# Kernel tuning notes

Measured on AMD Instinct MI355X. Metric: run time of the kernel, lower is better.

## Reference

```python
import jax, jax.numpy as jnp
import numpy as np

MAX_PER_CLASS = 100   # max_num_boxes_per_class
MAX_TOTAL = 300       # max_num_boxes (pad_per_class=False -> output size is MAX_TOTAL)
IOU_THR = 0.5
SCORE_THR = 0.001
NEG = jnp.float32(-1e30)
EPS = 1e-12


def _canon(b):
    # boxes given as any diagonal pair (y1,x1,y2,x2); canonicalize like TF NMS
    ymin = jnp.minimum(b[..., 0], b[..., 2])
    ymax = jnp.maximum(b[..., 0], b[..., 2])
    xmin = jnp.minimum(b[..., 1], b[..., 3])
    xmax = jnp.maximum(b[..., 1], b[..., 3])
    return ymin, xmin, ymax, xmax


def _iou_one_vs_all(box, boxes):
    # box [4], boxes [N,4] -> iou [N]
    y1a, x1a, y2a, x2a = _canon(box)
    y1b, x1b, y2b, x2b = _canon(boxes)
    ih = jnp.maximum(jnp.minimum(y2a, y2b) - jnp.maximum(y1a, y1b), 0.0)
    iw = jnp.maximum(jnp.minimum(x2a, x2b) - jnp.maximum(x1a, x1b), 0.0)
    inter = ih * iw
    area_a = (y2a - y1a) * (x2a - x1a)
    area_b = (y2b - y1b) * (x2b - x1b)
    union = jnp.maximum(area_a + area_b - inter, EPS)
    return inter / union


def _nms_single_class(boxes_c, scores_c):
    # boxes_c [N,4], scores_c [N] -> (scores [K], boxes [K,4], valid [K]) with K=MAX_PER_CLASS
    N = scores_c.shape[0]
    valid = scores_c > SCORE_THR
    s = jnp.where(valid, scores_c, NEG)
    order = jnp.argsort(-s)
    b_sorted = boxes_c[order]          # [N,4]
    s_sorted = s[order]                # [N]
    v_sorted = valid[order]            # [N]

    def step(keep, xs):
        i, box_i, valid_i = xs
        iou_row = _iou_one_vs_all(box_i, b_sorted)          # [N]
        suppressed = jnp.any(keep & (iou_row > IOU_THR))    # vs previously kept only
        keep = keep.at[i].set(valid_i & jnp.logical_not(suppressed))
        return keep, None

    keep0 = jnp.zeros((N,), dtype=bool)
    keep, _ = jax.lax.scan(step, keep0, (jnp.arange(N), b_sorted, v_sorted))

    # cap number of kept boxes at MAX_PER_CLASS (in descending score order)
    rank = jnp.cumsum(keep.astype(jnp.int32)) - 1
    keep = keep & (rank < MAX_PER_CLASS)

    key = jnp.where(keep, s_sorted, NEG)
    top_s, top_i = jax.lax.top_k(key, MAX_PER_CLASS)
    top_boxes = b_sorted[top_i]
    top_valid = top_s > (NEG / 2)
    return top_s, top_boxes, top_valid


def _combined_nms(scores, boxes):
    # scores [B,N,C], boxes [B,N,q,4] with q==1 (boxes shared across classes)
    B, N, C = scores.shape
    q = boxes.shape[2]

    def per_image(scores_i, boxes_i):
        # scores_i [N,C], boxes_i [N,q,4]
        if q == 1:
            cls_boxes = jnp.broadcast_to(boxes_i, (N, C, 4))
        else:
            cls_boxes = boxes_i
        # per-class NMS, vmapped over the class axis
        sc, bx, vd = jax.vmap(_nms_single_class, in_axes=(1, 1))(cls_boxes, scores_i)
        # sc [C,K], bx [C,K,4], vd [C,K]
        cls_ids = jnp.broadcast_to(
            jnp.arange(C, dtype=scores.dtype)[:, None], vd.shape)

        flat_s = jnp.where(vd, sc, NEG).reshape(-1)   # [C*K]
        flat_b = bx.reshape(-1, 4)
        flat_c = cls_ids.reshape(-1)
        flat_v = vd.reshape(-1)

        top_s, idx = jax.lax.top_k(flat_s, MAX_TOTAL)
        out_v = flat_v[idx]
        out_s = jnp.where(out_v, top_s, 0.0)
        out_b = jnp.where(out_v[:, None], flat_b[idx], 0.0)
        out_b = jnp.clip(out_b, 0.0, 1.0)             # clip_boxes=True
        out_c = jnp.where(out_v, flat_c[idx], 0.0)
        count = jnp.sum(out_v.astype(jnp.int32))
        return out_s, out_b, out_c, count

    return jax.vmap(per_image)(scores, boxes)


def setup_inputs() -> dict:
    key = jax.random.key(0)
    k1, k2 = jax.random.split(key)
    B, N, C, Q = 4, 1024, 80, 1
    scores = jax.random.uniform(k1, (B, N, C), dtype=jnp.float32)
    boxes = jax.random.uniform(k2, (B, N, Q, 4), dtype=jnp.float32)
    return {"scores": scores, "boxes": boxes}


def reference(scores, boxes):
    # returns (output_scores, output_boxes, output_classes, valid_counts)
    return _combined_nms(scores, boxes)
```

## Files before the change

### kernel.cpp

```cpp
#include <hip/hip_runtime.h>
#include <stdint.h>

#define N_BOX 1024
#define C_CLS 80
#define B_IMG 4
#define K_PER 100
#define K_TOT 300
#define NEGF  (-1e30f)
#define NWORD 16
#define NCAND (C_CLS * K_PER)
#define M_SEL 8192
#define KPAD  1088

#define OFF_SCOREST 0
#define OFF_MASKS   1310720
#define OFF_WSCORE  1835008
#define OFF_WSIDX   1963008

typedef unsigned long long u64;
typedef unsigned int u32;

__device__ __forceinline__ int swz(int i) { return i + (i >> 4); }

__device__ __forceinline__ u32 ford(float f) {
    u32 u = __float_as_uint(f);
    return (u & 0x80000000u) ? ~u : (u | 0x80000000u);
}
__device__ __forceinline__ float funord(u32 o) {
    u32 u = (o & 0x80000000u) ? (o ^ 0x80000000u) : ~o;
    return __uint_as_float(u);
}

__global__ __launch_bounds__(256) void prep_kernel(
        const float* __restrict__ scores,
        const float* __restrict__ boxes,
        u64*   __restrict__ masks,
        float* __restrict__ scoresT)
{
    __shared__ float4 bx[N_BOX];
    __shared__ float  ar[N_BOX];
    const int tid = threadIdx.x;

    if (blockIdx.x < 256) {
        const int b  = blockIdx.x >> 6;
        const int rg = blockIdx.x & 63;
        for (int n = tid; n < N_BOX; n += 256) {
            float4 v = ((const float4*)boxes)[b * N_BOX + n];
            {
#pragma clang fp contract(off)
                float y1 = fminf(v.x, v.z), y2 = fmaxf(v.x, v.z);
                float x1 = fminf(v.y, v.w), x2 = fmaxf(v.y, v.w);
                bx[n] = make_float4(y1, x1, y2, x2);
                ar[n] = (y2 - y1) * (x2 - x1);
            }
        }
        __syncthreads();

        const int r = tid >> 4;
        const int w = tid & 15;
        const int i = rg * 16 + r;
        const float4 a = bx[i];
        const float area_a = ar[i];
        u64 m = 0;
        const int j0 = w * 64;
        for (int jj = 0; jj < 64; ++jj) {
            int j = j0 + jj;
            float4 q = bx[j];
            {
#pragma clang fp contract(off)
                float ih = fminf(a.z, q.z) - fmaxf(a.x, q.x); ih = fmaxf(ih, 0.0f);
                float iw = fminf(a.w, q.w) - fmaxf(a.y, q.y); iw = fmaxf(iw, 0.0f);
                float inter = ih * iw;
                float uni = fmaxf(area_a + ar[j] - inter, 1e-12f);
                if (j != i && (inter / uni) > 0.5f) m |= (1ull << jj);
            }
        }
        masks[((size_t)(b * N_BOX + i)) * NWORD + w] = m;
    } else {
        float* tile = (float*)bx;
        const int t = blockIdx.x - 256;
        const int b  = t / 320;
        const int rm = t % 320;
        const int n0 = (rm / 5) * 16;
        const int c0 = (rm % 5) * 16;
        const int r = tid >> 4, cc = tid & 15;
        tile[r * 17 + cc] = scores[(size_t)(b * N_BOX + n0 + r) * C_CLS + c0 + cc];
        __syncthreads();
        scoresT[(size_t)(b * C_CLS + c0 + r) * N_BOX + n0 + cc] = tile[cc * 17 + r];
    }
}

__global__ __launch_bounds__(512) void nms_classes(
        const float* __restrict__ scoresT,
        const u64*   __restrict__ masks,
        float* __restrict__ ws_score,
        int*   __restrict__ ws_idx)
{
    __shared__ u64 key[2][KPAD];
    __shared__ u64 rows[2][64][NWORD];
    __shared__ int kept_t[2][K_PER];
    __shared__ int sh_nvalid[2], sh_kept[2];

    const int tid  = threadIdx.x;
    const int half = tid >> 8;
    const int lt   = tid & 255;
    const int lane = tid & 63;
    const int b  = blockIdx.x / (C_CLS / 2);
    const int c  = (blockIdx.x % (C_CLS / 2)) * 2 + half;

    if (lt == 0) { sh_nvalid[half] = 0; sh_kept[half] = 0; }
    __syncthreads();

    u64 r[4];
    {
        const float4 s4 = ((const float4*)(scoresT + ((size_t)(b * C_CLS + c) << 10)))[lt];
        float sv[4] = {s4.x, s4.y, s4.z, s4.w};
        int lv = 0;
        #pragma unroll
        for (int q = 0; q < 4; ++q) {
            bool valid = sv[q] > 0.001f;
            float s = valid ? sv[q] : NEGF;
            int v = lt * 4 + q;
            r[q] = ((u64)ford(s) << 32) | (u32)(N_BOX - 1 - v);
            lv += valid ? 1 : 0;
        }
        if (lv) atomicAdd(&sh_nvalid[half], lv);
    }

    #define CE(a, b, d) { u64 _mx = (a) > (b) ? (a) : (b); \
                          u64 _mn = (a) > (b) ? (b) : (a); \
                          (a) = (d) ? _mx : _mn; (b) = (d) ? _mn : _mx; }
    CE(r[0], r[1], true); CE(r[2], r[3], false);

    for (int k = 4; k <= N_BOX; k <<= 1) {
        const bool d = ((lt & (k >> 2)) == 0);
        for (int j = k >> 1; j > 0; j >>= 1) {
            if (j >= 256) {
                __syncthreads();
                #pragma unroll
                for (int q = 0; q < 4; ++q) key[half][swz(lt * 4 + q)] = r[q];
                __syncthreads();
                const bool upper = ((lt * 4) & j) != 0;
                #pragma unroll
                for (int q = 0; q < 4; ++q) {
                    u64 pv = key[half][swz((lt * 4 + q) ^ j)];
                    u64 mx = r[q] > pv ? r[q] : pv;
                    u64 mn = r[q] > pv ? pv : r[q];
                    r[q] = (d != upper) ? mx : mn;
                }
            } else if (j >= 4) {
                const int dl = j >> 2;
                const bool upper = (lane & dl) != 0;
                #pragma unroll
                for (int q = 0; q < 4; ++q) {
                    u64 pv = __shfl_xor(r[q], dl);
                    u64 mx = r[q] > pv ? r[q] : pv;
                    u64 mn = r[q] > pv ? pv : r[q];
                    r[q] = (d != upper) ? mx : mn;
                }
            } else if (j == 2) {
                CE(r[0], r[2], d); CE(r[1], r[3], d);
            } else {
                CE(r[0], r[1], d); CE(r[2], r[3], d);
            }
        }
    }
    #undef CE

    __syncthreads();
    #pragma unroll
    for (int q = 0; q < 4; ++q) key[half][swz(lt * 4 + q)] = r[q];
    __syncthreads();

    const int wv = tid >> 6;
    if (wv == 0 || wv == 4) {
        const int gh = wv >> 2;
        const int w16 = lane & 15;
        const int sslot = lane >> 4;
        const u64* mrow = masks + (size_t)b * N_BOX * NWORD;
        const int nvalid = sh_nvalid[gh];
        u64 sup = 0;
        int kept = 0;

        for (int bt = 0; bt < nvalid && kept < K_PER; bt += 64) {
            int t = bt + lane;
            bool in = t < nvalid;
            u64 kv = key[gh][swz(t & (N_BOX - 1))];
            int idx = (N_BOX - 1) - (int)(u32)(kv & 0xFFFFFFFFu);
            const int widx = idx >> 6, bidx = idx & 63;

            u64 supw = __shfl(sup, widx);
            bool sbit = (supw >> bidx) & 1ull;
            u64 pending = __ballot(in && !sbit);
            if (!pending) continue;

            #pragma unroll
            for (int p = 0; p < 16; ++p) {
                int rr = p * 4 + sslot;
                int ir = __shfl(idx, rr);
                u64 w = ((bt + rr) < nvalid) ? mrow[(size_t)ir * NWORD + w16] : 0;
                rows[gh][rr][w16] = w;
            }
            __builtin_amdgcn_wave_barrier();

            u64 kill_mask = 0;
            #pragma unroll
            for (int rr = 0; rr < 64; ++rr) {
                u64 w = rows[gh][rr][widx];
                kill_mask |= ((w >> bidx) & 1ull) << rr;
            }

            while (pending && kept < K_PER) {
                int t0 = __ffsll((long long)pending) - 1;
                if (lane == 0) kept_t[gh][kept] = bt + t0;
                kept++;
                if (lane < NWORD) sup |= rows[gh][t0][w16];
                bool kill = (kill_mask >> t0) & 1ull;
                pending &= ~(1ull << t0);
                pending &= ~__ballot(kill);
            }
        }
        if (lane == 0) sh_kept[gh] = kept;
    }
    __syncthreads();

    const int kept = sh_kept[half];
    if (lt < K_PER) {
        int ob = (b * C_CLS + c) * K_PER + lt;
        if (lt < kept) {
            u64 k = key[half][swz(kept_t[half][lt])];
            ws_score[ob] = funord((u32)(k >> 32));
            ws_idx[ob]   = (N_BOX - 1) - (int)(u32)(k & 0xFFFFFFFFu);
        } else {
            ws_score[ob] = NEGF;
            ws_idx[ob]   = 0;
        }
    }
}

__global__ __launch_bounds__(1024) void final_topk(
        const float* __restrict__ ws_score,
        const int*   __restrict__ ws_idx,
        const float* __restrict__ boxes,
        float* __restrict__ out)
{
    __shared__ u32 skey[NCAND];
    __shared__ u32 hist4[256 * 4];
    __shared__ u64 list[512];
    __shared__ int sh_sel;
    __shared__ u32 sh_need;
    __shared__ int sh_cnt, sh_valid;

    const int tid = threadIdx.x;
    const int b = blockIdx.x;
    const int base = b * NCAND;

    if (tid == 0) { sh_cnt = 0; sh_valid = 0; }
    for (int i = tid; i < NCAND; i += 1024)
        skey[i] = ford(ws_score[base + i]);
    if (tid < 512) list[tid] = 0;
    hist4[tid] = 0;
    __syncthreads();

    u64 prefix = 0;
    u32 need = K_TOT;
    const int rounds[6] = {7, 6, 5, 4, 1, 0};
    const int slot = tid & 3;

    for (int rd = 0; rd < 6; ++rd) {
        const int d = rounds[rd];
        for (int i = tid; i < NCAND; i += 1024) {
            u64 k = ((u64)skey[i] << 32) | (u32)(M_SEL - 1 - i);
            bool match = (d == 7) || (((k ^ prefix) >> (8 * (d + 1))) == 0);
            if (match)
                atomicAdd(&hist4[(((u32)(k >> (8 * d)) & 0xFFu) << 2) | slot], 1u);
        }
        __syncthreads();
        if (tid < 64) {
            const int l = tid;
            u32 h[4];
            #pragma unroll
            for (int q = 0; q < 4; ++q) {
                int bin = 4 * l + q;
                h[q] = hist4[bin * 4 + 0] + hist4[bin * 4 + 1]
                     + hist4[bin * 4 + 2] + hist4[bin * 4 + 3];
                hist4[bin * 4 + 0] = 0; hist4[bin * 4 + 1] = 0;
                hist4[bin * 4 + 2] = 0; hist4[bin * 4 + 3] = 0;
            }
            u32 s3 = h[3], s2 = h[2] + s3, s1 = h[1] + s2, s0 = h[0] + s1;
            u32 tot = s0, S = tot;
            #pragma unroll
            for (int off = 1; off < 64; off <<= 1) {
                u32 t = __shfl(S, (l + off) & 63);
                if (l + off < 64) S += t;
            }
            u32 T = S - tot;
            u32 sv0 = s0 + T, sv1 = s1 + T, sv2 = s2 + T, sv3 = s3 + T;
            if (sv0 >= need && sv1 < need) { sh_sel = 4*l;     sh_need = need - sv1; }
            if (sv1 >= need && sv2 < need) { sh_sel = 4*l + 1; sh_need = need - sv2; }
            if (sv2 >= need && sv3 < need) { sh_sel = 4*l + 2; sh_need = need - sv3; }
            if (sv3 >= need && T   < need) { sh_sel = 4*l + 3; sh_need = need - T;   }
        }
        __syncthreads();
        prefix |= ((u64)(u32)sh_sel) << (8 * d);
        need = sh_need;
        __syncthreads();
    }

    for (int i = tid; i < NCAND; i += 1024) {
        u64 k = ((u64)skey[i] << 32) | (u32)(M_SEL - 1 - i);
        if (k >= prefix) {
            int p = atomicAdd(&sh_cnt, 1);
            if (p < 512) list[p] = k;
        }
    }
    __syncthreads();

    if (tid < 64) {
        const int l = tid;
        u64 e[8];
        #pragma unroll
        for (int q = 0; q < 8; ++q) e[q] = list[l * 8 + q];
        #define CE2(a, b, dd) { u64 _mx = (a) > (b) ? (a) : (b); \
                                u64 _mn = (a) > (b) ? (b) : (a); \
                                (a) = (dd) ? _mx : _mn; (b) = (dd) ? _mn : _mx; }
        CE2(e[0], e[1], true);  CE2(e[2], e[3], false);
        CE2(e[4], e[5], true);  CE2(e[6], e[7], false);
        CE2(e[0], e[2], true);  CE2(e[1], e[3], true);
        CE2(e[4], e[6], false); CE2(e[5], e[7], false);
        CE2(e[0], e[1], true);  CE2(e[2], e[3], true);
        CE2(e[4], e[5], false); CE2(e[6], e[7], false);
        for (int k = 8; k <= 512; k <<= 1) {
            const bool d = ((l & (k >> 3)) == 0);
            for (int j = k >> 1; j >= 8; j >>= 1) {
                const int dl = j >> 3;
                const bool upper = (l & dl) != 0;
                #pragma unroll
                for (int q = 0; q < 8; ++q) {
                    u64 pv = __shfl_xor(e[q], dl);
                    u64 mx = e[q] > pv ? e[q] : pv;
                    u64 mn = e[q] > pv ? pv : e[q];
                    e[q] = (d != upper) ? mx : mn;
                }
            }
            CE2(e[0], e[4], d); CE2(e[1], e[5], d);
            CE2(e[2], e[6], d); CE2(e[3], e[7], d);
            CE2(e[0], e[2], d); CE2(e[1], e[3], d);
            CE2(e[4], e[6], d); CE2(e[5], e[7], d);
            CE2(e[0], e[1], d); CE2(e[2], e[3], d);
            CE2(e[4], e[5], d); CE2(e[6], e[7], d);
        }
        #undef CE2
        #pragma unroll
        for (int q = 0; q < 8; ++q) list[l * 8 + q] = e[q];
    }
    __syncthreads();

    float* out_s = out;
    float* out_b = out + B_IMG * K_TOT;
    float* out_c = out + B_IMG * K_TOT * 5;
    float* out_n = out + B_IMG * K_TOT * 6;

    for (int i = tid; i < K_TOT; i += 1024) {
        u64 k = list[i];
        float s = funord((u32)(k >> 32));
        int flat = (M_SEL - 1) - (int)(u32)(k & 0xFFFFFFFFu);
        bool valid = s > (-5e29f);
        float os = 0.0f, oc = 0.0f;
        float4 ob = make_float4(0.0f, 0.0f, 0.0f, 0.0f);
        if (valid && flat < NCAND) {
            int cc = flat / K_PER;
            int n  = ws_idx[base + flat];
            float4 bb = ((const float4*)boxes)[b * N_BOX + n];
            os = s;
            oc = (float)cc;
            ob.x = fminf(fmaxf(bb.x, 0.0f), 1.0f);
            ob.y = fminf(fmaxf(bb.y, 0.0f), 1.0f);
            ob.z = fminf(fmaxf(bb.z, 0.0f), 1.0f);
            ob.w = fminf(fmaxf(bb.w, 0.0f), 1.0f);
            atomicAdd(&sh_valid, 1);
        }
        out_s[b * K_TOT + i] = os;
        ((float4*)out_b)[b * K_TOT + i] = ob;
        out_c[b * K_TOT + i] = oc;
    }
    __syncthreads();
    if (tid == 0) out_n[b] = (float)sh_valid;
}

extern "C" void kernel_launch(void* const* d_in, const int* in_sizes, int n_in,
                              void* d_out, int out_size, void* d_ws, size_t ws_size,
                              hipStream_t stream) {
    const float* scores = (const float*)d_in[0];
    const float* boxes  = (const float*)d_in[1];

    char* ws = (char*)d_ws;
    float* scoresT  = (float*)(ws + OFF_SCOREST);
    u64*   masks    = (u64*)  (ws + OFF_MASKS);
    float* ws_score = (float*)(ws + OFF_WSCORE);
    int*   ws_idx   = (int*)  (ws + OFF_WSIDX);

    prep_kernel<<<dim3(256 + 1280), dim3(256), 0, stream>>>(scores, boxes, masks, scoresT);
    nms_classes<<<dim3(B_IMG * (C_CLS / 2)), dim3(512), 0, stream>>>(
        scoresT, masks, ws_score, ws_idx);
    final_topk<<<dim3(B_IMG), dim3(1024), 0, stream>>>(
        ws_score, ws_idx, boxes, (float*)d_out);
}
```

Before: 131.0 us.

## Precompute per-tile kill masks across all waves before serial NMS scan

Moves the gather of IoU mask rows and the 64x64 in-tile kill-mask construction out of the serial single-wave NMS loop. All four waves per class build these masks for every 64-box tile in parallel and store them in shared memory. The serial wave then only reads the precomputed mask and ORs suppression words for kept boxes, gathering them directly from global memory in batches of eight. This adds work for tiles the serial scan would have skipped and uses more shared memory, which may lower occupancy.

After: 141.0 us. 7.7% more time.

```diff
diff --git a/kernel.cpp b/kernel.cpp
--- a/kernel.cpp
+++ b/kernel.cpp
@@ -97,7 +97,8 @@
         int*   __restrict__ ws_idx)
 {
     __shared__ u64 key[2][KPAD];
-    __shared__ u64 rows[2][64][NWORD];
+    __shared__ u64 killm[2][16][64];
+    __shared__ u64 scratch[2][4][64][NWORD];
     __shared__ int kept_t[2][K_PER];
     __shared__ int sh_nvalid[2], sh_kept[2];
 
@@ -172,52 +173,86 @@
     for (int q = 0; q < 4; ++q) key[half][swz(lt * 4 + q)] = r[q];
     __syncthreads();
 
-    const int wv = tid >> 6;
-    if (wv == 0 || wv == 4) {
-        const int gh = wv >> 2;
-        const int w16 = lane & 15;
-        const int sslot = lane >> 4;
-        const u64* mrow = masks + (size_t)b * N_BOX * NWORD;
-        const int nvalid = sh_nvalid[gh];
-        u64 sup = 0;
-        int kept = 0;
-
-        for (int bt = 0; bt < nvalid && kept < K_PER; bt += 64) {
-            int t = bt + lane;
-            bool in = t < nvalid;
-            u64 kv = key[gh][swz(t & (N_BOX - 1))];
+    const u64* mrow = masks + (size_t)b * N_BOX * NWORD;
+    const int w16 = lane & 15;
+    const int sslot = lane >> 4;
+    const int nvalid = sh_nvalid[half];
+
+    {
+        const int wq = (tid >> 6) & 3;
+        for (int w = wq; w < 16; w += 4) {
+            const int bt = w * 64;
+            if (bt >= nvalid) break;
+            u64 kv = key[half][swz(bt + lane)];
             int idx = (N_BOX - 1) - (int)(u32)(kv & 0xFFFFFFFFu);
             const int widx = idx >> 6, bidx = idx & 63;
-
-            u64 supw = __shfl(sup, widx);
-            bool sbit = (supw >> bidx) & 1ull;
-            u64 pending = __ballot(in && !sbit);
-            if (!pending) continue;
-
             #pragma unroll
             for (int p = 0; p < 16; ++p) {
                 int rr = p * 4 + sslot;
                 int ir = __shfl(idx, rr);
-                u64 w = ((bt + rr) < nvalid) ? mrow[(size_t)ir * NWORD + w16] : 0;
-                rows[gh][rr][w16] = w;
+                u64 v = ((bt + rr) < nvalid) ? mrow[(size_t)ir * NWORD + w16] : 0;
+                scratch[half][wq][rr][w16] = v;
             }
             __builtin_amdgcn_wave_barrier();
-
-            u64 kill_mask = 0;
+            u64 km = 0;
             #pragma unroll
-            for (int rr = 0; rr < 64; ++rr) {
-                u64 w = rows[gh][rr][widx];
-                kill_mask |= ((w >> bidx) & 1ull) << rr;
-            }
+            for (int rr = 0; rr < 64; ++rr)
+                km |= ((scratch[half][wq][rr][widx] >> bidx) & 1ull) << rr;
+            killm[half][w][lane] = km;
+            __builtin_amdgcn_wave_barrier();
+        }
+    }
+    __syncthreads();
+
+    const int wv = tid >> 6;
+    if (wv == 0 || wv == 4) {
+        const int gh = wv >> 2;
+        const int nv = sh_nvalid[gh];
+        u64 sup = 0;
+        int kept = 0;
+
+        for (int w = 0; w < 16 && kept < K_PER; ++w) {
+            const int bt = w * 64;
+            if (bt >= nv) break;
+            bool in = (bt + lane) < nv;
+            u64 kv = key[gh][swz(bt + lane)];
+            int idx = (N_BOX - 1) - (int)(u32)(kv & 0xFFFFFFFFu);
+            const int widx = idx >> 6, bidx = idx & 63;
+            u64 supw = __shfl(sup, widx);
+            u64 pending = __ballot(in && !((supw >> bidx) & 1ull));
+            if (!pending) continue;
+            u64 km = killm[gh][w][lane];
+            u64 accmask = 0;
 
             while (pending && kept < K_PER) {
                 int t0 = __ffsll((long long)pending) - 1;
                 if (lane == 0) kept_t[gh][kept] = bt + t0;
                 kept++;
-                if (lane < NWORD) sup |= rows[gh][t0][w16];
-                bool kill = (kill_mask >> t0) & 1ull;
+                accmask |= (1ull << t0);
+                bool kill = (km >> t0) & 1ull;
                 pending &= ~(1ull << t0);
                 pending &= ~__ballot(kill);
+            }
+
+            while (accmask) {
+                int ia[8]; int n = 0;
+                #pragma unroll
+                for (int r2 = 0; r2 < 8; ++r2) {
+                    ia[r2] = 0;
+                    if (accmask) {
+                        int a = __ffsll((long long)accmask) - 1;
+                        accmask &= accmask - 1;
+                        ia[r2] = __shfl(idx, a);
+                        n = r2 + 1;
+                    }
+                }
+                u64 vv[8];
+                #pragma unroll
+                for (int r2 = 0; r2 < 8; ++r2)
+                    vv[r2] = (r2 < n && lane < NWORD)
+                           ? mrow[(size_t)ia[r2] * NWORD + w16] : 0;
+                #pragma unroll
+                for (int r2 = 0; r2 < 8; ++r2) sup |= vv[r2];
             }
         }
         if (lane == 0) sh_kept[gh] = kept;
```
